# Optimization experiments

Hardware: AMD Instinct MI355X
Metric: run time of the kernel (lower is better)

Reference implementation:

```python
import jax, jax.numpy as jnp
import numpy as np

FACTOR = 5  # init factor


def setup_inputs() -> dict:
    key = jax.random.key(0)
    k1, k2, k3, k4 = jax.random.split(key, 4)
    B, H, L, D = 4, 8, 2048, 64
    sample_k = min(FACTOR * int(np.ceil(np.log(L))), L)  # 40
    queries = jax.random.normal(k1, (B, H, L, D), dtype=jnp.float32)
    keys = jax.random.normal(k2, (B, H, L, D), dtype=jnp.float32)
    values = jax.random.normal(k3, (B, H, L, D), dtype=jnp.float32)
    index_sample = jax.random.randint(k4, (L, sample_k), 0, L)
    return {"queries": queries, "keys": keys, "values": values,
            "index_sample": index_sample}


def reference(queries, keys, values, index_sample):
    B, H, L_Q, D = queries.shape
    L_K = keys.shape[2]
    n_top = min(FACTOR * int(np.ceil(np.log(L_Q))), L_Q)

    # --- _prob_QK ---
    # Gather sampled keys per query position: [B,H,L_Q,sample_k,D]
    K_sample = keys[:, :, index_sample, :]
    # Q.unsqueeze(3) @ K_sample^T -> [B,H,L_Q,sample_k]
    Q_K_sample = jnp.einsum('bhld,bhlsd->bhls', queries, K_sample)
    # sparsity measure M = max - mean
    M = Q_K_sample.max(axis=-1) - Q_K_sample.sum(axis=-1) / L_K
    _, M_top = jax.lax.top_k(M, n_top)  # [B,H,n_top]
    # gather top queries: [B,H,n_top,D]
    Q_reduce = jnp.take_along_axis(queries, M_top[..., None], axis=2)
    # full scores for top queries: [B,H,n_top,L_K]
    scores_top = jnp.einsum('bhud,bhkd->bhuk', Q_reduce, keys)

    # --- scale ---
    scale = 1.0 / np.sqrt(D).astype(np.float32)
    scores_top = scores_top * scale

    # --- initial context (mask_flag=False): mean of V broadcast over L_Q ---
    V_mean = values.mean(axis=2)  # [B,H,D]
    context = jnp.broadcast_to(V_mean[:, :, None, :], (B, H, L_Q, D))

    # --- update context at top-query positions ---
    attn = jax.nn.softmax(scores_top, axis=-1)           # [B,H,n_top,L_K]
    ctx_update = jnp.einsum('bhuk,bhkd->bhud', attn, values)
    b_idx = jnp.arange(B)[:, None, None]
    h_idx = jnp.arange(H)[None, :, None]
    context = context.at[b_idx, h_idx, M_top].set(ctx_update)
    return context
```

## Files before the change

kernel.cpp:

```cpp
#include <hip/hip_runtime.h>
#include <math.h>

#define BH 32
#define L  2048
#define D  64
#define SK 40
#define NT 40
#define NC 16
#define CK 128
#define SP 129
#define SCALE 0.125f

#define WS_M      0
#define WS_MTOP   262144
#define WS_VP     267264
#define WS_VM     529408
#define WS_QTOP   537600
#define WS_OPART  865280
#define WS_MPART  6108160
#define WS_LPART  6190080

template <int CTRL>
__device__ __forceinline__ float dpp_add(float x) {
    int y = __builtin_amdgcn_update_dpp(0, __float_as_int(x), CTRL, 0xF, 0xF, true);
    return x + __int_as_float(y);
}

__global__ __launch_bounds__(512) void kMV(const float* __restrict__ Q,
                                           const float* __restrict__ K,
                                           const float* __restrict__ V,
                                           const int* __restrict__ idx,
                                           float* __restrict__ M,
                                           float* __restrict__ Vp)
{
    __shared__ int   sidx[64 * SK];
    __shared__ float red[512];

    int t    = threadIdx.x;
    int b    = blockIdx.x;
    int head = ((b >> 3) & 3) * 8 + (b & 7);
    int qc   = b >> 5;
    int l0   = qc * 64;

    {
        int d = t & 63, r = t >> 6;
        const float* Vb = V + ((size_t)head * L + l0 + r * 8) * D + d;
        float acc = 0.f;
        #pragma unroll
        for (int k = 0; k < 8; ++k) acc += Vb[(size_t)k * D];
        red[t] = acc;
    }
    for (int i = t; i < 64 * SK; i += 512) sidx[i] = idx[l0 * SK + i];
    __syncthreads();
    if (t < 64) {
        float s = 0.f;
        #pragma unroll
        for (int rr = 0; rr < 8; ++rr) s += red[t + rr * 64];
        Vp[(head * 32 + qc) * 64 + t] = s;
    }

    int wave = t >> 6, lane = t & 63;
    int g  = lane >> 3;
    int dl = lane & 7;
    int lq = wave * 8 + g;
    size_t qid = (size_t)head * L + (l0 + lq);

    const float4* Q4 = reinterpret_cast<const float4*>(Q);
    float4 q0 = Q4[qid * 16 + dl * 2 + 0];
    float4 q1 = Q4[qid * 16 + dl * 2 + 1];
    const float4* Kb4 = reinterpret_cast<const float4*>(K) + (size_t)head * L * 16;

    float mx = -INFINITY, sm = 0.f;
    #pragma unroll 4
    for (int s = 0; s < SK; ++s) {
        int kr = sidx[lq * SK + s];
        const float4* kp = Kb4 + (size_t)kr * 16 + dl * 2;
        float4 k0 = kp[0], k1 = kp[1];
        float p = q0.x * k0.x + q0.y * k0.y + q0.z * k0.z + q0.w * k0.w
                + q1.x * k1.x + q1.y * k1.y + q1.z * k1.z + q1.w * k1.w;
        p = dpp_add<0xB1>(p);
        p = dpp_add<0x4E>(p);
        p = dpp_add<0x12C>(p);
        mx = fmaxf(mx, p);
        sm += p;
    }
    if (dl == 0) M[qid] = mx - sm * (1.0f / (float)L);
}

__global__ __launch_bounds__(256) void kTopVm(const float* __restrict__ M,
                                              const float* __restrict__ Vp,
                                              const float* __restrict__ Q,
                                              int* __restrict__ Mtop,
                                              float* __restrict__ Vm,
                                              float* __restrict__ Qtop)
{
    __shared__ unsigned int keys[L];
    __shared__ int hist[256];
    __shared__ int ssum[256];
    __shared__ int bsel;
    __shared__ unsigned int pref_s;
    __shared__ int krem_s;
    __shared__ int cnt_gt, cnt_eq;
    __shared__ int eqlist[64];
    __shared__ int stop[NT];

    int bh = blockIdx.x;
    int t  = threadIdx.x;

    if (t < 64) {
        float s = 0.f;
        #pragma unroll
        for (int c = 0; c < 32; ++c) s += Vp[(bh * 32 + c) * 64 + t];
        Vm[bh * D + t] = s * (1.0f / (float)L);
    }

    for (int i = t; i < L; i += 256) {
        unsigned int u = __float_as_uint(M[bh * L + i]);
        keys[i] = (u & 0x80000000u) ? ~u : (u | 0x80000000u);
    }
    if (t == 0) { pref_s = 0u; krem_s = NT; cnt_gt = 0; cnt_eq = 0; }
    __syncthreads();

    #pragma unroll
    for (int shift = 24; shift >= 0; shift -= 8) {
        hist[t] = 0;
        __syncthreads();
        unsigned int pref = pref_s;
        for (int i = t; i < L; i += 256) {
            unsigned int k  = keys[i];
            unsigned int hi = (shift == 24) ? 0u : (k >> (shift + 8));
            if (hi == pref) atomicAdd(&hist[(k >> shift) & 0xFF], 1);
        }
        __syncthreads();
        ssum[t] = hist[t];
        __syncthreads();
        for (int st = 1; st < 256; st <<= 1) {
            int v = (t + st < 256) ? ssum[t + st] : 0;
            __syncthreads();
            ssum[t] += v;
            __syncthreads();
        }
        int krem = krem_s;
        int excl = ssum[t] - hist[t];
        if (excl < krem && excl + hist[t] >= krem) bsel = t;
        __syncthreads();
        if (t == 0) {
            int bb = bsel;
            krem_s = krem_s - (ssum[bb] - hist[bb]);
            pref_s = (pref_s << 8) | (unsigned int)bb;
        }
        __syncthreads();
    }

    unsigned int T = pref_s;
    int krem = krem_s;
    for (int i = t; i < L; i += 256) {
        unsigned int k = keys[i];
        if (k > T) {
            int p = atomicAdd(&cnt_gt, 1);
            Mtop[bh * NT + p] = i;
            stop[p] = i;
        } else if (k == T) {
            int p = atomicAdd(&cnt_eq, 1);
            if (p < 64) eqlist[p] = i;
        }
    }
    __syncthreads();
    if (t == 0) {
        int base = cnt_gt;
        int m = cnt_eq < 64 ? cnt_eq : 64;
        for (int q = 0; q < krem; ++q) {
            int best = 0x7fffffff, bj = -1;
            for (int j = 0; j < m; ++j) if (eqlist[j] < best) { best = eqlist[j]; bj = j; }
            Mtop[bh * NT + base + q] = best;
            stop[base + q] = best;
            if (bj >= 0) eqlist[bj] = 0x7fffffff;
        }
    }
    __syncthreads();
    const float4* Qg = reinterpret_cast<const float4*>(Q) + (size_t)bh * L * 16;
    float4* Qt = reinterpret_cast<float4*>(Qtop) + (size_t)bh * NT * 16;
    for (int i = t; i < NT * 16; i += 256)
        Qt[i] = Qg[(size_t)stop[i >> 4] * 16 + (i & 15)];
}

__global__ __launch_bounds__(256, 2) void kAttnPart(const float* __restrict__ Qtop,
                                                    const float* __restrict__ K,
                                                    const float* __restrict__ V,
                                                    const float* __restrict__ Vm,
                                                    float* __restrict__ Opart,
                                                    float* __restrict__ mpart,
                                                    float* __restrict__ lpart,
                                                    float* __restrict__ out)
{
    __shared__ float4 V4[CK * 16];
    __shared__ float  S[NT * SP];
    __shared__ float  smax[NT], ssum[NT];

    int c = blockIdx.x, bh = blockIdx.y;
    int t = threadIdx.x;

    {
        const float4* Vm4 = reinterpret_cast<const float4*>(Vm + bh * D);
        float4* outB = reinterpret_cast<float4*>(out) + ((size_t)bh * L + c * CK) * 16;
        #pragma unroll
        for (int k = 0; k < 8; ++k) { int i = t + k * 256; outB[i] = Vm4[i & 15]; }
    }

    const float4* Vg = reinterpret_cast<const float4*>(V) + ((size_t)bh * L + c * CK) * 16;
    float4 vreg[8];
    #pragma unroll
    for (int k = 0; k < 8; ++k) vreg[k] = Vg[t + k * 256];

    int w    = __builtin_amdgcn_readfirstlane(t) >> 6;
    int lane = t & 63;
    const float4* Kg = reinterpret_cast<const float4*>(K) + ((size_t)bh * L + c * CK) * 16;
    float4 k0[16], k1[16];
    #pragma unroll
    for (int d4 = 0; d4 < 16; ++d4) {
        k0[d4] = Kg[(size_t)lane * 16 + d4];
        k1[d4] = Kg[(size_t)(64 + lane) * 16 + d4];
    }

    const float* Qb = Qtop + ((size_t)bh * NT + w * 10) * D;
    float p0[10], p1[10];
    #pragma unroll
    for (int i = 0; i < 10; ++i) {
        const float* qrow = Qb + i * D;
        float a0 = 0.f, a1 = 0.f;
        #pragma unroll
        for (int d4 = 0; d4 < 16; ++d4) {
            float4 q4 = *reinterpret_cast<const float4*>(qrow + d4 * 4);
            a0 += q4.x * k0[d4].x + q4.y * k0[d4].y + q4.z * k0[d4].z + q4.w * k0[d4].w;
            a1 += q4.x * k1[d4].x + q4.y * k1[d4].y + q4.z * k1[d4].z + q4.w * k1[d4].w;
        }
        p0[i] = a0 * SCALE; p1[i] = a1 * SCALE;
    }

    #pragma unroll
    for (int i = 0; i < 10; ++i) {
        int u = w * 10 + i;
        float m = fmaxf(p0[i], p1[i]);
        #pragma unroll
        for (int o = 1; o < 64; o <<= 1) m = fmaxf(m, __shfl_xor(m, o, 64));
        float e0 = __expf(p0[i] - m), e1 = __expf(p1[i] - m);
        float l2 = e0 + e1;
        #pragma unroll
        for (int o = 1; o < 64; o <<= 1) l2 += __shfl_xor(l2, o, 64);
        S[u * SP + lane]      = e0;
        S[u * SP + 64 + lane] = e1;
        if (lane == 0) { smax[u] = m; ssum[u] = l2; }
    }

    #pragma unroll
    for (int k = 0; k < 8; ++k) {
        int i = t + k * 256;
        int j = i >> 4, d4 = i & 15;
        V4[j * 16 + (d4 ^ (j & 15))] = vreg[k];
    }
    __syncthreads();

    {
        int a = t >> 5, r = t & 31;
        int d4 = r >> 1, jh = r & 1;
        float4 acc[5];
        #pragma unroll
        for (int ui = 0; ui < 5; ++ui) acc[ui] = make_float4(0.f, 0.f, 0.f, 0.f);
        for (int jj = 0; jj < 64; ++jj) {
            int j = jh * 64 + jj;
            float4 v4 = V4[j * 16 + (d4 ^ (j & 15))];
            #pragma unroll
            for (int ui = 0; ui < 5; ++ui) {
                float p = S[(a + 8 * ui) * SP + j];
                acc[ui].x += p * v4.x; acc[ui].y += p * v4.y;
                acc[ui].z += p * v4.z; acc[ui].w += p * v4.w;
            }
        }
        #pragma unroll
        for (int ui = 0; ui < 5; ++ui) {
            acc[ui].x = dpp_add<0xB1>(acc[ui].x);
            acc[ui].y = dpp_add<0xB1>(acc[ui].y);
            acc[ui].z = dpp_add<0xB1>(acc[ui].z);
            acc[ui].w = dpp_add<0xB1>(acc[ui].w);
        }
        if (jh == 0) {
            float4* Og = reinterpret_cast<float4*>(Opart) + ((size_t)(bh * NC + c) * NT) * 16;
            #pragma unroll
            for (int ui = 0; ui < 5; ++ui)
                Og[(a + 8 * ui) * 16 + d4] = acc[ui];
        }
    }
    if (t < NT) {
        mpart[(bh * NC + c) * NT + t] = smax[t];
        lpart[(bh * NC + c) * NT + t] = ssum[t];
    }
}

__global__ __launch_bounds__(64) void kCombine(const float* __restrict__ Opart,
                                               const float* __restrict__ mpart,
                                               const float* __restrict__ lpart,
                                               const int* __restrict__ Mtop,
                                               float* __restrict__ out)
{
    int u = blockIdx.x, bh = blockIdx.y, d = threadIdx.x;
    float gm = -INFINITY, den = 0.f, o = 0.f;
    for (int c = 0; c < NC; ++c) {
        int pi = (bh * NC + c) * NT + u;
        float mv = mpart[pi], lv = lpart[pi];
        float nm = fmaxf(gm, mv);
        float r1 = __expf(gm - nm), r2 = __expf(mv - nm);
        o   = o * r1 + r2 * Opart[(size_t)pi * D + d];
        den = den * r1 + r2 * lv;
        gm  = nm;
    }
    int qrow = Mtop[bh * NT + u];
    out[((size_t)bh * L + qrow) * D + d] = o / den;
}

extern "C" void kernel_launch(void* const* d_in, const int* in_sizes, int n_in,
                              void* d_out, int out_size, void* d_ws, size_t ws_size,
                              hipStream_t stream)
{
    const float* Q   = (const float*)d_in[0];
    const float* K   = (const float*)d_in[1];
    const float* V   = (const float*)d_in[2];
    const int*   idx = (const int*)d_in[3];
    float* out = (float*)d_out;

    char* ws = (char*)d_ws;
    float* M     = (float*)(ws + WS_M);
    int*   Mtop  = (int*)  (ws + WS_MTOP);
    float* Vp    = (float*)(ws + WS_VP);
    float* Vm    = (float*)(ws + WS_VM);
    float* Qtop  = (float*)(ws + WS_QTOP);
    float* Opart = (float*)(ws + WS_OPART);
    float* mpart = (float*)(ws + WS_MPART);
    float* lpart = (float*)(ws + WS_LPART);

    kMV      <<<1024, 512, 0, stream>>>(Q, K, V, idx, M, Vp);
    kTopVm   <<<BH, 256, 0, stream>>>(M, Vp, Q, Mtop, Vm, Qtop);
    kAttnPart<<<dim3(NC, BH), 256, 0, stream>>>(Qtop, K, V, Vm, Opart, mpart, lpart, out);
    kCombine <<<dim3(NT, BH), 64, 0, stream>>>(Opart, mpart, lpart, Mtop, out);
}
```

Measured before the change: 165.5 us.

## Fuse top-k selection and combine into producer kernels via last-block atomic counters

Merges the top-k selection kernel into the score kernel and the combine kernel into the partial-attention kernel. A per-head atomic counter lets the last finishing block of each group run the follow-up stage. This removes two kernel launches and their inter-kernel gaps at the cost of a tiny init kernel, thread fences, and a serial tail that runs inside one block per head. The top-k stage now uses 512 threads with guards for the 256-wide histogram logic.

```diff
diff --git a/kernel.cpp b/kernel.cpp
--- a/kernel.cpp
+++ b/kernel.cpp
@@ -19,6 +19,7 @@
 #define WS_OPART  865280
 #define WS_MPART  6108160
 #define WS_LPART  6190080
+#define WS_CNT    6272000
 
 template <int CTRL>
 __device__ __forceinline__ float dpp_add(float x) {
@@ -26,12 +27,18 @@
     return x + __int_as_float(y);
 }
 
-__global__ __launch_bounds__(512) void kMV(const float* __restrict__ Q,
-                                           const float* __restrict__ K,
-                                           const float* __restrict__ V,
-                                           const int* __restrict__ idx,
-                                           float* __restrict__ M,
-                                           float* __restrict__ Vp)
+__global__ void kInit(unsigned int* __restrict__ cnt) { cnt[threadIdx.x] = 0u; }
+
+__global__ __launch_bounds__(512) void kMVTop(const float* __restrict__ Q,
+                                              const float* __restrict__ K,
+                                              const float* __restrict__ V,
+                                              const int* __restrict__ idx,
+                                              float* __restrict__ M,
+                                              float* __restrict__ Vp,
+                                              int* __restrict__ Mtop,
+                                              float* __restrict__ Vm,
+                                              float* __restrict__ Qtop,
+                                              unsigned int* __restrict__ cnt1)
 {
     __shared__ int   sidx[64 * SK];
     __shared__ float red[512];
@@ -85,15 +92,15 @@
         sm += p;
     }
     if (dl == 0) M[qid] = mx - sm * (1.0f / (float)L);
-}
-
-__global__ __launch_bounds__(256) void kTopVm(const float* __restrict__ M,
-                                              const float* __restrict__ Vp,
-                                              const float* __restrict__ Q,
-                                              int* __restrict__ Mtop,
-                                              float* __restrict__ Vm,
-                                              float* __restrict__ Qtop)
-{
+
+    __threadfence();
+    __syncthreads();
+    __shared__ unsigned int lastflag;
+    if (t == 0) lastflag = (atomicAdd(&cnt1[head], 1u) == 31u) ? 1u : 0u;
+    __syncthreads();
+    if (!lastflag) return;
+    __threadfence();
+
     __shared__ unsigned int keys[L];
     __shared__ int hist[256];
     __shared__ int ssum[256];
@@ -103,9 +110,7 @@
     __shared__ int cnt_gt, cnt_eq;
     __shared__ int eqlist[64];
     __shared__ int stop[NT];
-
-    int bh = blockIdx.x;
-    int t  = threadIdx.x;
+    int bh = head;
 
     if (t < 64) {
         float s = 0.f;
@@ -113,8 +118,7 @@
         for (int c = 0; c < 32; ++c) s += Vp[(bh * 32 + c) * 64 + t];
         Vm[bh * D + t] = s * (1.0f / (float)L);
     }
-
-    for (int i = t; i < L; i += 256) {
+    for (int i = t; i < L; i += 512) {
         unsigned int u = __float_as_uint(M[bh * L + i]);
         keys[i] = (u & 0x80000000u) ? ~u : (u | 0x80000000u);
     }
@@ -123,26 +127,28 @@
 
     #pragma unroll
     for (int shift = 24; shift >= 0; shift -= 8) {
-        hist[t] = 0;
+        if (t < 256) hist[t] = 0;
         __syncthreads();
         unsigned int pref = pref_s;
-        for (int i = t; i < L; i += 256) {
+        for (int i = t; i < L; i += 512) {
             unsigned int k  = keys[i];
             unsigned int hi = (shift == 24) ? 0u : (k >> (shift + 8));
             if (hi == pref) atomicAdd(&hist[(k >> shift) & 0xFF], 1);
         }
         __syncthreads();
-        ssum[t] = hist[t];
+        if (t < 256) ssum[t] = hist[t];
         __syncthreads();
         for (int st = 1; st < 256; st <<= 1) {
-            int v = (t + st < 256) ? ssum[t + st] : 0;
+            int v = (t < 256 && t + st < 256) ? ssum[t + st] : 0;
             __syncthreads();
-            ssum[t] += v;
+            if (t < 256) ssum[t] += v;
             __syncthreads();
         }
-        int krem = krem_s;
-        int excl = ssum[t] - hist[t];
-        if (excl < krem && excl + hist[t] >= krem) bsel = t;
+        if (t < 256) {
+            int krem = krem_s;
+            int excl = ssum[t] - hist[t];
+            if (excl < krem && excl + hist[t] >= krem) bsel = t;
+        }
         __syncthreads();
         if (t == 0) {
             int bb = bsel;
@@ -154,7 +160,7 @@
 
     unsigned int T = pref_s;
     int krem = krem_s;
-    for (int i = t; i < L; i += 256) {
+    for (int i = t; i < L; i += 512) {
         unsigned int k = keys[i];
         if (k > T) {
             int p = atomicAdd(&cnt_gt, 1);
@@ -180,7 +186,7 @@
     __syncthreads();
     const float4* Qg = reinterpret_cast<const float4*>(Q) + (size_t)bh * L * 16;
     float4* Qt = reinterpret_cast<float4*>(Qtop) + (size_t)bh * NT * 16;
-    for (int i = t; i < NT * 16; i += 256)
+    for (int i = t; i < NT * 16; i += 512)
         Qt[i] = Qg[(size_t)stop[i >> 4] * 16 + (i & 15)];
 }
 
@@ -188,10 +194,12 @@
                                                     const float* __restrict__ K,
                                                     const float* __restrict__ V,
                                                     const float* __restrict__ Vm,
+                                                    const int* __restrict__ Mtop,
                                                     float* __restrict__ Opart,
                                                     float* __restrict__ mpart,
                                                     float* __restrict__ lpart,
-                                                    float* __restrict__ out)
+                                                    float* __restrict__ out,
+                                                    unsigned int* __restrict__ cnt2)
 {
     __shared__ float4 V4[CK * 16];
     __shared__ float  S[NT * SP];
@@ -294,27 +302,30 @@
         mpart[(bh * NC + c) * NT + t] = smax[t];
         lpart[(bh * NC + c) * NT + t] = ssum[t];
     }
-}
-
-__global__ __launch_bounds__(64) void kCombine(const float* __restrict__ Opart,
-                                               const float* __restrict__ mpart,
-                                               const float* __restrict__ lpart,
-                                               const int* __restrict__ Mtop,
-                                               float* __restrict__ out)
-{
-    int u = blockIdx.x, bh = blockIdx.y, d = threadIdx.x;
-    float gm = -INFINITY, den = 0.f, o = 0.f;
-    for (int c = 0; c < NC; ++c) {
-        int pi = (bh * NC + c) * NT + u;
-        float mv = mpart[pi], lv = lpart[pi];
-        float nm = fmaxf(gm, mv);
-        float r1 = __expf(gm - nm), r2 = __expf(mv - nm);
-        o   = o * r1 + r2 * Opart[(size_t)pi * D + d];
-        den = den * r1 + r2 * lv;
-        gm  = nm;
-    }
-    int qrow = Mtop[bh * NT + u];
-    out[((size_t)bh * L + qrow) * D + d] = o / den;
+
+    __threadfence();
+    __syncthreads();
+    __shared__ unsigned int lastf;
+    if (t == 0) lastf = (atomicAdd(&cnt2[bh], 1u) == (unsigned int)(NC - 1)) ? 1u : 0u;
+    __syncthreads();
+    if (!lastf) return;
+    __threadfence();
+
+    int d = t & 63;
+    for (int u = t >> 6; u < NT; u += 4) {
+        float gm = -INFINITY, den = 0.f, o = 0.f;
+        for (int cc = 0; cc < NC; ++cc) {
+            int pi = (bh * NC + cc) * NT + u;
+            float mv = mpart[pi], lv = lpart[pi];
+            float nm = fmaxf(gm, mv);
+            float r1 = __expf(gm - nm), r2 = __expf(mv - nm);
+            o   = o * r1 + r2 * Opart[(size_t)pi * D + d];
+            den = den * r1 + r2 * lv;
+            gm  = nm;
+        }
+        int qrow = Mtop[bh * NT + u];
+        out[((size_t)bh * L + qrow) * D + d] = o / den;
+    }
 }
 
 extern "C" void kernel_launch(void* const* d_in, const int* in_sizes, int n_in,
@@ -336,9 +347,10 @@
     float* Opart = (float*)(ws + WS_OPART);
     float* mpart = (float*)(ws + WS_MPART);
     float* lpart = (float*)(ws + WS_LPART);
-
-    kMV      <<<1024, 512, 0, stream>>>(Q, K, V, idx, M, Vp);
-    kTopVm   <<<BH, 256, 0, stream>>>(M, Vp, Q, Mtop, Vm, Qtop);
-    kAttnPart<<<dim3(NC, BH), 256, 0, stream>>>(Qtop, K, V, Vm, Opart, mpart, lpart, out);
-    kCombine <<<dim3(NT, BH), 64, 0, stream>>>(Opart, mpart, lpart, Mtop, out);
+    unsigned int* cnt = (unsigned int*)(ws + WS_CNT);
+
+    kInit    <<<1, 64, 0, stream>>>(cnt);
+    kMVTop   <<<1024, 512, 0, stream>>>(Q, K, V, idx, M, Vp, Mtop, Vm, Qtop, cnt);
+    kAttnPart<<<dim3(NC, BH), 256, 0, stream>>>(Qtop, K, V, Vm, Mtop,
+                                                Opart, mpart, lpart, out, cnt + 32);
 }
```

New measurement: 421.5 us. 155% more time.
